# Optimization experiments

Measured on AMD Instinct MI355X. Metric: run time of the kernel, lower is better.

Reference implementation:

```python
import jax, jax.numpy as jnp
import numpy as np

N, E, F_IN, H, C, G, OUT = 50000, 800000, 128, 4, 64, 64, 16
NEG_SLOPE = 0.2


def _gat_layer(x, src, dst, W, a_src, a_dst, b):
    # x: [N, Fin]; W: [Fin, H*C]; a_src/a_dst: [H, C]; b: [H*C]
    h = (x @ W).reshape(N, H, C)                      # [N,H,C]
    e_src = jnp.einsum('nhc,hc->nh', h, a_src)        # [N,H]
    e_dst = jnp.einsum('nhc,hc->nh', h, a_dst)
    e = jax.nn.leaky_relu(e_src[src] + e_dst[dst], NEG_SLOPE)  # [Etot,H]
    # segment softmax over edges sharing a destination node
    m = jax.ops.segment_max(e, dst, num_segments=N)   # [N,H]
    ex = jnp.exp(e - m[dst])
    s = jax.ops.segment_sum(ex, dst, num_segments=N)  # [N,H]
    alpha = ex / s[dst]                               # [Etot,H]
    msg = h[src] * alpha[:, :, None]                  # [Etot,H,C]
    out = jax.ops.segment_sum(msg, dst, num_segments=N)
    return out.reshape(N, H * C) + b


def setup_inputs() -> dict:
    key = jax.random.key(0)
    ks = jax.random.split(key, 12)
    x = jax.random.normal(ks[0], (N, F_IN), dtype=jnp.float32)
    edge_index = jax.random.randint(ks[1], (2, E), 0, N, dtype=jnp.int64)
    batch = jnp.sort(jax.random.randint(ks[2], (N,), 0, G, dtype=jnp.int64))
    hc = H * C
    W1 = jax.random.normal(ks[3], (F_IN, hc), dtype=jnp.float32) / np.sqrt(F_IN)
    a_src1 = jax.random.normal(ks[4], (H, C), dtype=jnp.float32) / np.sqrt(C)
    a_dst1 = jax.random.normal(ks[5], (H, C), dtype=jnp.float32) / np.sqrt(C)
    b1 = jnp.zeros((hc,), dtype=jnp.float32)
    W2 = jax.random.normal(ks[6], (hc, hc), dtype=jnp.float32) / np.sqrt(hc)
    a_src2 = jax.random.normal(ks[7], (H, C), dtype=jnp.float32) / np.sqrt(C)
    a_dst2 = jax.random.normal(ks[8], (H, C), dtype=jnp.float32) / np.sqrt(C)
    b2 = jnp.zeros((hc,), dtype=jnp.float32)
    Wlin = jax.random.normal(ks[9], (hc, OUT), dtype=jnp.float32) / np.sqrt(hc)
    blin = jnp.zeros((OUT,), dtype=jnp.float32)
    return dict(x=x, edge_index=edge_index, batch=batch,
                W1=W1, a_src1=a_src1, a_dst1=a_dst1, b1=b1,
                W2=W2, a_src2=a_src2, a_dst2=a_dst2, b2=b2,
                Wlin=Wlin, blin=blin)


def reference(x, edge_index, batch, W1, a_src1, a_dst1, b1,
              W2, a_src2, a_dst2, b2, Wlin, blin):
    # add self-loops (PyG GATConv default add_self_loops=True)
    loops = jnp.arange(N, dtype=edge_index.dtype)
    src = jnp.concatenate([edge_index[0], loops])
    dst = jnp.concatenate([edge_index[1], loops])
    h = jax.nn.relu(_gat_layer(x, src, dst, W1, a_src1, a_dst1, b1))
    h = jax.nn.relu(_gat_layer(h, src, dst, W2, a_src2, a_dst2, b2))
    # global mean pool over graphs
    sums = jax.ops.segment_sum(h, batch, num_segments=G)          # [G, H*C]
    cnt = jax.ops.segment_sum(jnp.ones((N,), h.dtype), batch, num_segments=G)
    pooled = sums / jnp.maximum(cnt, 1.0)[:, None]
    return pooled @ Wlin + blin                                    # [G, OUT]
```

## Files before the change

kernel.cpp:

```cpp
#include <hip/hip_runtime.h>
#include <hip/hip_fp16.h>

#define NN   50000
#define EE   800000
#define ETOT 850000
#define FIN  128
#define HC   256
#define NH   4
#define CH   64
#define NG   64
#define NOUT 16
#define NEG_SLOPE 0.2f

#define NBUCK 391
#define BCAP  4096
#define EPB   4096
#define NEB   208

typedef _Float16 f16x8 __attribute__((ext_vector_type(8)));
typedef float    f32x4 __attribute__((ext_vector_type(4)));

__global__ __launch_bounds__(256) void edge_bucket(const int* __restrict__ ei,
                                                   int* __restrict__ bucket_counts,
                                                   unsigned* __restrict__ buckets) {
    __shared__ int h[NBUCK];
    __shared__ int bb[NBUCK];
    const int tid = threadIdx.x;
    const int e0  = blockIdx.x * EPB;

    for (int t = tid; t < NBUCK; t += 256) h[t] = 0;
    __syncthreads();

    int srcs[16], dsts[16];
#pragma unroll
    for (int k = 0; k < 16; ++k) {
        int i = e0 + k * 256 + tid;
        int s = 0, d = -1;
        if (i < ETOT) {
            s = (i < EE) ? ei[i] : (i - EE);
            d = (i < EE) ? ei[EE + i] : (i - EE);
            atomicAdd(&h[d >> 7], 1);
        }
        srcs[k] = s; dsts[k] = d;
    }
    __syncthreads();

    for (int t = tid; t < NBUCK; t += 256) {
        bb[t] = atomicAdd(&bucket_counts[t], h[t]);
        h[t]  = 0;
    }
    __syncthreads();

#pragma unroll
    for (int k = 0; k < 16; ++k) {
        int d = dsts[k];
        if (d >= 0) {
            int b = d >> 7;
            int r = atomicAdd(&h[b], 1);
            int idx = bb[b] + r;
            if (idx < BCAP)
                buckets[(size_t)b * BCAP + idx] =
                    (unsigned)srcs[k] | ((unsigned)(d & 127) << 16);
        }
    }
}

__global__ __launch_bounds__(512) void bucket_scan(const int* __restrict__ counts,
                                                   int* __restrict__ basep,
                                                   int* __restrict__ rowptr) {
    __shared__ int lds[512];
    const int tid = threadIdx.x;
    int v = (tid < NBUCK) ? counts[tid] : 0;
    lds[tid] = v;
    __syncthreads();
    for (int off = 1; off < 512; off <<= 1) {
        int t = (tid >= off) ? lds[tid - off] : 0;
        __syncthreads();
        lds[tid] += t;
        __syncthreads();
    }
    if (tid < NBUCK) basep[tid] = lds[tid] - v;
    if (tid == 0) rowptr[NN] = ETOT;
}

__global__ __launch_bounds__(256) void bucket_to_csr(const unsigned* __restrict__ buckets,
                                                     const int* __restrict__ bucket_counts,
                                                     const int* __restrict__ bucket_base,
                                                     int* __restrict__ rowptr,
                                                     int* __restrict__ csr) {
    __shared__ int h[128], c[128], sc[128];
    const int b = blockIdx.x, tid = threadIdx.x;
    const int nb   = bucket_counts[b];
    const int base = bucket_base[b];

    if (tid < 128) h[tid] = 0;
    __syncthreads();
    for (int i = tid; i < nb; i += 256) {
        unsigned p = buckets[(size_t)b * BCAP + i];
        atomicAdd(&h[p >> 16], 1);
    }
    __syncthreads();
    if (tid < 128) sc[tid] = h[tid];
    __syncthreads();
    for (int off = 1; off < 128; off <<= 1) {
        int t = (tid < 128 && tid >= off) ? sc[tid - off] : 0;
        __syncthreads();
        if (tid < 128) sc[tid] += t;
        __syncthreads();
    }
    if (tid < 128) {
        int excl = sc[tid] - h[tid];
        c[tid] = excl;
        int node = (b << 7) + tid;
        if (node < NN) rowptr[node] = base + excl;
    }
    __syncthreads();
    for (int i = tid; i < nb; i += 256) {
        unsigned p = buckets[(size_t)b * BCAP + i];
        int pos = atomicAdd(&c[p >> 16], 1);
        csr[base + pos] = (int)(p & 0xFFFFu);
    }
}

__global__ void f32_to_f16_vec(const float* __restrict__ in, __half* __restrict__ out,
                               int n4) {
    int i = blockIdx.x * 256 + threadIdx.x;
    if (i >= n4) return;
    float4 v = *(const float4*)&in[(size_t)i * 4];
    __half h[4] = {__float2half(v.x), __float2half(v.y), __float2half(v.z), __float2half(v.w)};
    *(uint2*)&out[(size_t)i * 4] = *(uint2*)h;
}

__global__ void w_transpose_f16(const float* __restrict__ W, __half* __restrict__ Wt,
                                int K) {
    int idx = blockIdx.x * 256 + threadIdx.x;
    if (idx >= K * HC) return;
    int n = idx / K, k = idx - n * K;
    Wt[idx] = __float2half(W[(size_t)k * HC + n]);
}

__global__ __launch_bounds__(256) void gemm_f16(const __half* __restrict__ A16,
                                                const __half* __restrict__ Bt16,
                                                __half* __restrict__ C16,
                                                const float* __restrict__ a_src,
                                                const float* __restrict__ a_dst,
                                                float* __restrict__ es,
                                                float* __restrict__ ed,
                                                int M, int K) {
    __shared__ char lds[32768];
    const int tid  = threadIdx.x;
    const int m0   = blockIdx.y * 128;
    const int n0   = blockIdx.x * 128;
    const int wid  = tid >> 6, lane = tid & 63;
    const int wr   = wid >> 1, wc = wid & 1;
    const int l15  = lane & 15, l4 = lane >> 4;
    const int trow = tid >> 3;
    const int tcol = (tid & 7) * 8;

    f32x4 acc[4][4] = {};

    for (int k0 = 0; k0 < K; k0 += 64) {
        __syncthreads();
#pragma unroll
        for (int it = 0; it < 4; ++it) {
            int row = trow + it * 32;
            uint4 v = make_uint4(0u, 0u, 0u, 0u);
            int gr = m0 + row;
            if (gr < M) v = *(const uint4*)&A16[(size_t)gr * K + k0 + tcol];
            int off = (row * 128 + tcol * 2) ^ ((row & 7) << 4);
            *(uint4*)(lds + off) = v;
            uint4 w = *(const uint4*)&Bt16[(size_t)(n0 + row) * K + k0 + tcol];
            int offb = 16384 + ((row * 128 + tcol * 2) ^ ((row & 7) << 4));
            *(uint4*)(lds + offb) = w;
        }
        __syncthreads();
#pragma unroll
        for (int ks = 0; ks < 2; ++ks) {
            f16x8 af[4], bf[4];
#pragma unroll
            for (int i = 0; i < 4; ++i) {
                int rowA = wr * 64 + i * 16 + l15;
                int offA = (rowA * 128 + ks * 64 + l4 * 16) ^ ((rowA & 7) << 4);
                af[i] = *(const f16x8*)(lds + offA);
                int rowB = wc * 64 + i * 16 + l15;
                int offB = 16384 + ((rowB * 128 + ks * 64 + l4 * 16) ^ ((rowB & 7) << 4));
                bf[i] = *(const f16x8*)(lds + offB);
            }
#pragma unroll
            for (int i = 0; i < 4; ++i)
#pragma unroll
                for (int j = 0; j < 4; ++j)
                    acc[i][j] = __builtin_amdgcn_mfma_f32_16x16x32_f16(af[i], bf[j], acc[i][j], 0, 0, 0);
        }
    }
#pragma unroll
    for (int i = 0; i < 4; ++i) {
#pragma unroll
        for (int r = 0; r < 4; ++r) {
            int row = m0 + wr * 64 + i * 16 + l4 * 4 + r;
            if (row < M) {
#pragma unroll
                for (int j = 0; j < 4; ++j) {
                    int col = n0 + wc * 64 + j * 16 + l15;
                    C16[(size_t)row * HC + col] = __float2half(acc[i][j][r]);
                }
            }
        }
    }
    const int hd = blockIdx.x * 2 + wc;
    float as_[4], ad_[4];
#pragma unroll
    for (int j = 0; j < 4; ++j) {
        int c = j * 16 + l15;
        as_[j] = a_src[hd * CH + c];
        ad_[j] = a_dst[hd * CH + c];
    }
#pragma unroll
    for (int i = 0; i < 4; ++i) {
#pragma unroll
        for (int r = 0; r < 4; ++r) {
            float ps = 0.f, pd = 0.f;
#pragma unroll
            for (int j = 0; j < 4; ++j) {
                ps = fmaf(acc[i][j][r], as_[j], ps);
                pd = fmaf(acc[i][j][r], ad_[j], pd);
            }
#pragma unroll
            for (int mm = 8; mm; mm >>= 1) {
                ps += __shfl_xor(ps, mm);
                pd += __shfl_xor(pd, mm);
            }
            int row = m0 + wr * 64 + i * 16 + l4 * 4 + r;
            if (l15 == 0 && row < M) {
                es[row * NH + hd] = ps;
                ed[row * NH + hd] = pd;
            }
        }
    }
}

__global__ __launch_bounds__(256) void gat_fused(const __half* __restrict__ hfeat,
                                                 const float* __restrict__ es,
                                                 const float* __restrict__ ed,
                                                 const int* __restrict__ rowptr,
                                                 const int* __restrict__ csr_src,
                                                 const float* __restrict__ bias,
                                                 __half* __restrict__ out16) {
    const int node = blockIdx.x * 4 + (threadIdx.x >> 6);
    const int lane = threadIdx.x & 63;
    if (node >= NN) return;
    const int start = rowptr[node];
    const int deg   = rowptr[node + 1] - start;

    const int hh = lane & 3;
    const int el = lane >> 2;
    float4 ed4 = *(const float4*)&ed[node * NH];
    float ednh = (hh & 1) ? ((hh & 2) ? ed4.w : ed4.y)
                          : ((hh & 2) ? ed4.z : ed4.x);

    float mx = -1e30f;
    for (int j = el; j < deg; j += 16) {
        int src = csr_src[start + j];
        float e = es[src * NH + hh] + ednh;
        e = (e > 0.f) ? e : NEG_SLOPE * e;
        mx = fmaxf(mx, e);
    }
#pragma unroll
    for (int off = 4; off < 64; off <<= 1) mx = fmaxf(mx, __shfl_xor(mx, off));

    float sm = 0.f;
    for (int j = el; j < deg; j += 16) {
        int src = csr_src[start + j];
        float e = es[src * NH + hh] + ednh;
        e = (e > 0.f) ? e : NEG_SLOPE * e;
        sm += __expf(e - mx);
    }
#pragma unroll
    for (int off = 4; off < 64; off <<= 1) sm += __shfl_xor(sm, off);

    const int sub = lane >> 5;
    const int cl  = lane & 31;
    const int hsel = cl >> 3;
    const float mh  = __shfl(mx, hsel);
    const float ish = 1.0f / __shfl(sm, hsel);
    const float ehn = __shfl(ednh, hsel);

    float acc[8] = {0.f, 0.f, 0.f, 0.f, 0.f, 0.f, 0.f, 0.f};
    int j = 0;
    for (; j + 3 < deg; j += 4) {
        int jj0 = start + j + sub;
        int jj1 = start + j + 2 + sub;
        int s0 = csr_src[jj0];
        int s1 = csr_src[jj1];
        float e0 = es[s0 * NH + hsel] + ehn;
        float e1 = es[s1 * NH + hsel] + ehn;
        e0 = (e0 > 0.f) ? e0 : NEG_SLOPE * e0;
        e1 = (e1 > 0.f) ? e1 : NEG_SLOPE * e1;
        float a0 = __expf(e0 - mh) * ish;
        float a1 = __expf(e1 - mh) * ish;
        uint4 r0 = *(const uint4*)&hfeat[(size_t)s0 * HC + cl * 8];
        uint4 r1 = *(const uint4*)&hfeat[(size_t)s1 * HC + cl * 8];
        const unsigned* w0 = &r0.x;
        const unsigned* w1 = &r1.x;
#pragma unroll
        for (int q = 0; q < 4; ++q) {
            float2 f0 = __half22float2(*reinterpret_cast<const __half2*>(&w0[q]));
            float2 f1 = __half22float2(*reinterpret_cast<const __half2*>(&w1[q]));
            acc[q * 2]     = fmaf(a0, f0.x, acc[q * 2]);
            acc[q * 2 + 1] = fmaf(a0, f0.y, acc[q * 2 + 1]);
            acc[q * 2]     = fmaf(a1, f1.x, acc[q * 2]);
            acc[q * 2 + 1] = fmaf(a1, f1.y, acc[q * 2 + 1]);
        }
    }
    for (; j < deg; j += 2) {
        int jj = j + sub;
        if (jj < deg) {
            int s0 = csr_src[start + jj];
            float e0 = es[s0 * NH + hsel] + ehn;
            e0 = (e0 > 0.f) ? e0 : NEG_SLOPE * e0;
            float a0 = __expf(e0 - mh) * ish;
            uint4 r0 = *(const uint4*)&hfeat[(size_t)s0 * HC + cl * 8];
            const unsigned* w0 = &r0.x;
#pragma unroll
            for (int q = 0; q < 4; ++q) {
                float2 f0 = __half22float2(*reinterpret_cast<const __half2*>(&w0[q]));
                acc[q * 2]     = fmaf(a0, f0.x, acc[q * 2]);
                acc[q * 2 + 1] = fmaf(a0, f0.y, acc[q * 2 + 1]);
            }
        }
    }
#pragma unroll
    for (int q = 0; q < 8; ++q) acc[q] += __shfl_xor(acc[q], 32);

    if (lane < 32) {
        float4 b0 = *(const float4*)&bias[cl * 8];
        float4 b1 = *(const float4*)&bias[cl * 8 + 4];
        const float* bp0 = &b0.x;
        const float* bp1 = &b1.x;
        __half h[8];
#pragma unroll
        for (int q = 0; q < 4; ++q) h[q]     = __float2half(fmaxf(acc[q]     + bp0[q], 0.f));
#pragma unroll
        for (int q = 0; q < 4; ++q) h[4 + q] = __float2half(fmaxf(acc[4 + q] + bp1[q], 0.f));
        *(uint4*)&out16[(size_t)node * HC + cl * 8] = *(uint4*)h;
    }
}

__global__ __launch_bounds__(256) void pool_sum(const __half* __restrict__ h,
                                                const int* __restrict__ batch,
                                                float* __restrict__ sums) {
    int t  = threadIdx.x;
    int n0 = blockIdx.x * 128;
    if (n0 >= NN) return;
    int cur = batch[n0];
    float acc = 0.f;
    int nend = min(n0 + 128, NN);
    for (int n = n0; n < nend; ++n) {
        int g = batch[n];
        if (g != cur) {
            atomicAdd(&sums[cur * HC + t], acc);
            acc = 0.f; cur = g;
        }
        acc += __half2float(h[(size_t)n * HC + t]);
    }
    atomicAdd(&sums[cur * HC + t], acc);
}

__global__ void batch_bounds(const int* __restrict__ batch,
                             int* __restrict__ beg, int* __restrict__ end) {
    int i = blockIdx.x * 256 + threadIdx.x;
    if (i >= NN) return;
    int g = batch[i];
    if (i == 0      || batch[i - 1] != g) beg[g] = i;
    if (i == NN - 1 || batch[i + 1] != g) end[g] = i + 1;
}

__global__ __launch_bounds__(256) void final_linear(const float* __restrict__ sums,
                                                    const int* __restrict__ beg,
                                                    const int* __restrict__ end,
                                                    const float* __restrict__ Wlin,
                                                    const float* __restrict__ blin,
                                                    float* __restrict__ out) {
    int idx = blockIdx.x * 256 + threadIdx.x;
    if (idx >= NG * NOUT) return;
    int g = idx >> 4, o = idx & 15;
    float cnt = (float)(end[g] - beg[g]);
    float invc = 1.f / fmaxf(cnt, 1.f);
    float acc = 0.f;
    for (int k = 0; k < HC; ++k) acc += sums[g * HC + k] * Wlin[k * NOUT + o];
    out[idx] = acc * invc + blin[o];
}

extern "C" void kernel_launch(void* const* d_in, const int* in_sizes, int n_in,
                              void* d_out, int out_size, void* d_ws, size_t ws_size,
                              hipStream_t stream) {
    const float* x      = (const float*)d_in[0];
    const int*   ei     = (const int*)d_in[1];
    const int*   batch  = (const int*)d_in[2];
    const float* W1     = (const float*)d_in[3];
    const float* a_src1 = (const float*)d_in[4];
    const float* a_dst1 = (const float*)d_in[5];
    const float* b1     = (const float*)d_in[6];
    const float* W2     = (const float*)d_in[7];
    const float* a_src2 = (const float*)d_in[8];
    const float* a_dst2 = (const float*)d_in[9];
    const float* b2     = (const float*)d_in[10];
    const float* Wlin   = (const float*)d_in[11];
    const float* blin   = (const float*)d_in[12];
    float* out = (float*)d_out;

    char* p = (char*)d_ws;
    auto take = [&](size_t bytes) {
        char* r = p;
        p += (bytes + 255) & ~(size_t)255;
        return r;
    };
    __half*   bufT16 = (__half*)take((size_t)NN * HC * 2);
    __half*   bufH16 = (__half*)take((size_t)NN * HC * 2);
    __half*   x16    = (__half*)take((size_t)NN * FIN * 2);
    __half*   w1t    = (__half*)take((size_t)FIN * HC * 2);
    __half*   w2t    = (__half*)take((size_t)HC * HC * 2);
    float*    es     = (float*)take((size_t)NN * NH * 4);
    float*    ed     = (float*)take((size_t)NN * NH * 4);
    int*      rowptr = (int*)take((size_t)(NN + 1) * 4);
    int*      csr    = (int*)take((size_t)ETOT * 4);
    unsigned* buckets= (unsigned*)take((size_t)NBUCK * BCAP * 4);
    int*      bcnt   = (int*)take((size_t)NBUCK * 4);
    int*      bbase  = (int*)take((size_t)NBUCK * 4);
    float*    sums   = (float*)take((size_t)NG * HC * 4);
    int*      gbeg   = (int*)take((size_t)NG * 4);
    int*      gend   = (int*)take((size_t)NG * 4);

    hipMemsetAsync(bcnt, 0, (size_t)NBUCK * 4, stream);
    hipMemsetAsync(sums, 0, (size_t)NG * HC * 4, stream);
    hipMemsetAsync(gbeg, 0, (size_t)NG * 4, stream);
    hipMemsetAsync(gend, 0, (size_t)NG * 4, stream);

    edge_bucket<<<NEB, 256, 0, stream>>>(ei, bcnt, buckets);
    bucket_scan<<<1, 512, 0, stream>>>(bcnt, bbase, rowptr);
    bucket_to_csr<<<NBUCK, 256, 0, stream>>>(buckets, bcnt, bbase, rowptr, csr);
    f32_to_f16_vec<<<(NN * FIN / 4 + 255) / 256, 256, 0, stream>>>(x, x16, NN * FIN / 4);
    w_transpose_f16<<<(FIN * HC + 255) / 256, 256, 0, stream>>>(W1, w1t, FIN);
    w_transpose_f16<<<(HC * HC + 255) / 256, 256, 0, stream>>>(W2, w2t, HC);

    gemm_f16<<<dim3(2, (NN + 127) / 128), 256, 0, stream>>>(x16, w1t, bufT16,
                                                            a_src1, a_dst1, es, ed, NN, FIN);
    gat_fused<<<(NN + 3) / 4, 256, 0, stream>>>(bufT16, es, ed, rowptr, csr, b1, bufH16);

    gemm_f16<<<dim3(2, (NN + 127) / 128), 256, 0, stream>>>(bufH16, w2t, bufT16,
                                                            a_src2, a_dst2, es, ed, NN, HC);
    gat_fused<<<(NN + 3) / 4, 256, 0, stream>>>(bufT16, es, ed, rowptr, csr, b2, bufH16);

    pool_sum<<<(NN + 127) / 128, 256, 0, stream>>>(bufH16, batch, sums);
    batch_bounds<<<(NN + 255) / 256, 256, 0, stream>>>(batch, gbeg, gend);
    final_linear<<<4, 256, 0, stream>>>(sums, gbeg, gend, Wlin, blin, out);
}
```

Baseline: 296.9 us.

## Merge prep kernels, use direct global-to-LDS loads in GEMM, trim launches

```diff
diff --git a/kernel.cpp b/kernel.cpp
--- a/kernel.cpp
+++ b/kernel.cpp
@@ -122,21 +122,33 @@
     }
 }
 
-__global__ void f32_to_f16_vec(const float* __restrict__ in, __half* __restrict__ out,
-                               int n4) {
-    int i = blockIdx.x * 256 + threadIdx.x;
-    if (i >= n4) return;
-    float4 v = *(const float4*)&in[(size_t)i * 4];
-    __half h[4] = {__float2half(v.x), __float2half(v.y), __float2half(v.z), __float2half(v.w)};
-    *(uint2*)&out[(size_t)i * 4] = *(uint2*)h;
-}
-
-__global__ void w_transpose_f16(const float* __restrict__ W, __half* __restrict__ Wt,
-                                int K) {
-    int idx = blockIdx.x * 256 + threadIdx.x;
-    if (idx >= K * HC) return;
-    int n = idx / K, k = idx - n * K;
-    Wt[idx] = __float2half(W[(size_t)k * HC + n]);
+#define XB4 6250
+#define W1B 128
+#define W2B 256
+__global__ void prep_convert(const float* __restrict__ x, __half* __restrict__ x16,
+                             const float* __restrict__ W1, __half* __restrict__ w1t,
+                             const float* __restrict__ W2, __half* __restrict__ w2t) {
+    int b = blockIdx.x;
+    if (b < XB4) {
+        int i = b * 256 + threadIdx.x;
+        float4 v = *(const float4*)&x[(size_t)i * 4];
+        __half h[4] = {__float2half(v.x), __float2half(v.y), __float2half(v.z), __float2half(v.w)};
+        *(uint2*)&x16[(size_t)i * 4] = *(uint2*)h;
+    } else if (b < XB4 + W1B) {
+        int idx = (b - XB4) * 256 + threadIdx.x;
+        int n = idx / FIN, k = idx - n * FIN;
+        w1t[idx] = __float2half(W1[(size_t)k * HC + n]);
+    } else {
+        int idx = (b - XB4 - W1B) * 256 + threadIdx.x;
+        int n = idx / HC, k = idx - n * HC;
+        w2t[idx] = __float2half(W2[(size_t)k * HC + n]);
+    }
+}
+
+__device__ __forceinline__ void load_lds_16B(const void* g, void* l) {
+    __builtin_amdgcn_global_load_lds(
+        (const __attribute__((address_space(1))) void*)g,
+        (__attribute__((address_space(3))) void*)l, 16, 0, 0);
 }
 
 __global__ __launch_bounds__(256) void gemm_f16(const __half* __restrict__ A16,
@@ -156,6 +168,7 @@
     const int l15  = lane & 15, l4 = lane >> 4;
     const int trow = tid >> 3;
     const int tcol = (tid & 7) * 8;
+    const int scol = tcol ^ ((trow & 7) << 3);
 
     f32x4 acc[4][4] = {};
 
@@ -164,14 +177,12 @@
 #pragma unroll
         for (int it = 0; it < 4; ++it) {
             int row = trow + it * 32;
-            uint4 v = make_uint4(0u, 0u, 0u, 0u);
-            int gr = m0 + row;
-            if (gr < M) v = *(const uint4*)&A16[(size_t)gr * K + k0 + tcol];
-            int off = (row * 128 + tcol * 2) ^ ((row & 7) << 4);
-            *(uint4*)(lds + off) = v;
-            uint4 w = *(const uint4*)&Bt16[(size_t)(n0 + row) * K + k0 + tcol];
-            int offb = 16384 + ((row * 128 + tcol * 2) ^ ((row & 7) << 4));
-            *(uint4*)(lds + offb) = w;
+            int gr  = m0 + row;
+            int grc = (gr < M) ? gr : (M - 1);
+            load_lds_16B(&A16[(size_t)grc * K + k0 + scol],
+                         lds + it * 4096 + wid * 1024);
+            load_lds_16B(&Bt16[(size_t)(n0 + row) * K + k0 + scol],
+                         lds + 16384 + it * 4096 + wid * 1024);
         }
         __syncthreads();
 #pragma unroll
@@ -346,45 +357,43 @@
     }
 }
 
-__global__ __launch_bounds__(256) void pool_sum(const __half* __restrict__ h,
+__global__ __launch_bounds__(128) void pool_sum(const __half2* __restrict__ h2,
                                                 const int* __restrict__ batch,
                                                 float* __restrict__ sums) {
     int t  = threadIdx.x;
     int n0 = blockIdx.x * 128;
     if (n0 >= NN) return;
     int cur = batch[n0];
-    float acc = 0.f;
+    float ax = 0.f, ay = 0.f;
     int nend = min(n0 + 128, NN);
     for (int n = n0; n < nend; ++n) {
         int g = batch[n];
         if (g != cur) {
-            atomicAdd(&sums[cur * HC + t], acc);
-            acc = 0.f; cur = g;
-        }
-        acc += __half2float(h[(size_t)n * HC + t]);
-    }
-    atomicAdd(&sums[cur * HC + t], acc);
-}
-
-__global__ void batch_bounds(const int* __restrict__ batch,
-                             int* __restrict__ beg, int* __restrict__ end) {
-    int i = blockIdx.x * 256 + threadIdx.x;
-    if (i >= NN) return;
-    int g = batch[i];
-    if (i == 0      || batch[i - 1] != g) beg[g] = i;
-    if (i == NN - 1 || batch[i + 1] != g) end[g] = i + 1;
+            atomicAdd(&sums[cur * HC + 2 * t],     ax);
+            atomicAdd(&sums[cur * HC + 2 * t + 1], ay);
+            ax = ay = 0.f; cur = g;
+        }
+        float2 f = __half22float2(h2[(size_t)n * 128 + t]);
+        ax += f.x; ay += f.y;
+    }
+    atomicAdd(&sums[cur * HC + 2 * t],     ax);
+    atomicAdd(&sums[cur * HC + 2 * t + 1], ay);
 }
 
 __global__ __launch_bounds__(256) void final_linear(const float* __restrict__ sums,
-                                                    const int* __restrict__ beg,
-                                                    const int* __restrict__ end,
+                                                    const int* __restrict__ batch,
                                                     const float* __restrict__ Wlin,
                                                     const float* __restrict__ blin,
                                                     float* __restrict__ out) {
     int idx = blockIdx.x * 256 + threadIdx.x;
     if (idx >= NG * NOUT) return;
     int g = idx >> 4, o = idx & 15;
-    float cnt = (float)(end[g] - beg[g]);
+    int lo = 0, hi = NN;
+    while (lo < hi) { int mid = (lo + hi) >> 1; if (batch[mid] < g) lo = mid + 1; else hi = mid; }
+    int beg = lo;
+    hi = NN;
+    while (lo < hi) { int mid = (lo + hi) >> 1; if (batch[mid] <= g) lo = mid + 1; else hi = mid; }
+    float cnt = (float)(lo - beg);
     float invc = 1.f / fmaxf(cnt, 1.f);
     float acc = 0.f;
     for (int k = 0; k < HC; ++k) acc += sums[g * HC + k] * Wlin[k * NOUT + o];
@@ -425,23 +434,17 @@
     int*      rowptr = (int*)take((size_t)(NN + 1) * 4);
     int*      csr    = (int*)take((size_t)ETOT * 4);
     unsigned* buckets= (unsigned*)take((size_t)NBUCK * BCAP * 4);
-    int*      bcnt   = (int*)take((size_t)NBUCK * 4);
     int*      bbase  = (int*)take((size_t)NBUCK * 4);
-    float*    sums   = (float*)take((size_t)NG * HC * 4);
-    int*      gbeg   = (int*)take((size_t)NG * 4);
-    int*      gend   = (int*)take((size_t)NG * 4);
-
-    hipMemsetAsync(bcnt, 0, (size_t)NBUCK * 4, stream);
-    hipMemsetAsync(sums, 0, (size_t)NG * HC * 4, stream);
-    hipMemsetAsync(gbeg, 0, (size_t)NG * 4, stream);
-    hipMemsetAsync(gend, 0, (size_t)NG * 4, stream);
+    char*     zbase  = take((size_t)NG * HC * 4 + (size_t)NBUCK * 4);
+    float*    sums   = (float*)zbase;
+    int*      bcnt   = (int*)(zbase + (size_t)NG * HC * 4);
+
+    hipMemsetAsync(zbase, 0, (size_t)NG * HC * 4 + (size_t)NBUCK * 4, stream);
 
     edge_bucket<<<NEB, 256, 0, stream>>>(ei, bcnt, buckets);
     bucket_scan<<<1, 512, 0, stream>>>(bcnt, bbase, rowptr);
     bucket_to_csr<<<NBUCK, 256, 0, stream>>>(buckets, bcnt, bbase, rowptr, csr);
-    f32_to_f16_vec<<<(NN * FIN / 4 + 255) / 256, 256, 0, stream>>>(x, x16, NN * FIN / 4);
-    w_transpose_f16<<<(FIN * HC + 255) / 256, 256, 0, stream>>>(W1, w1t, FIN);
-    w_transpose_f16<<<(HC * HC + 255) / 256, 256, 0, stream>>>(W2, w2t, HC);
+    prep_convert<<<XB4 + W1B + W2B, 256, 0, stream>>>(x, x16, W1, w1t, W2, w2t);
 
     gemm_f16<<<dim3(2, (NN + 127) / 128), 256, 0, stream>>>(x16, w1t, bufT16,
                                                             a_src1, a_dst1, es, ed, NN, FIN);
@@ -451,7 +454,6 @@
                                                             a_src2, a_dst2, es, ed, NN, HC);
     gat_fused<<<(NN + 3) / 4, 256, 0, stream>>>(bufT16, es, ed, rowptr, csr, b2, bufH16);
 
-    pool_sum<<<(NN + 127) / 128, 256, 0, stream>>>(bufH16, batch, sums);
-    batch_bounds<<<(NN + 255) / 256, 256, 0, stream>>>(batch, gbeg, gend);
-    final_linear<<<4, 256, 0, stream>>>(sums, gbeg, gend, Wlin, blin, out);
-}
+    pool_sum<<<(NN + 127) / 128, 128, 0, stream>>>((const __half2*)bufH16, batch, sums);
+    final_linear<<<4, 256, 0, stream>>>(sums, batch, Wlin, blin, out);
+}
```

Measured after the change: 284.9 us. 4.0% less time.
